# Performance work log

Measured on AMD Instinct MI355X. Metric: run time of the kernel, lower is better.

Reference implementation:

```python
import jax, jax.numpy as jnp
import numpy as np

N_CYCLES = 20000  # number of cycles in the cycle basis (segments)


def setup_inputs() -> dict:
    key = jax.random.key(0)
    k1, k2, k3, k4, k5 = jax.random.split(key, 5)
    B, NB, E = 256, 50000, 160000  # batch, n_branches, total cycle-basis entries
    c = jax.random.normal(k1, (B, NB), dtype=jnp.float32)
    s = jax.random.normal(k2, (B, NB), dtype=jnp.float32)
    # signs are +/-1
    cysigns = jnp.where(jax.random.uniform(k4, (E,)) < 0.5, -1.0, 1.0).astype(jnp.float32)
    cyinds = jax.random.randint(k3, (E,), 0, NB, dtype=jnp.int32)
    # from_value_rowids requires nondecreasing row ids
    cyrows = jnp.sort(jax.random.randint(k5, (E,), 0, N_CYCLES, dtype=jnp.int32))
    return {"c": c, "s": s, "cysigns": cysigns, "cyinds": cyinds, "cyrows": cyrows}


def reference(c, s, cysigns, cyinds, cyrows):
    # gather branch vars per cycle-basis entry: [B, E]
    cg = jnp.take(c, cyinds, axis=1)
    sg = cysigns * jnp.take(s, cyinds, axis=1)
    # tf.math.angle(tf.complex(rc, rs)) == atan2(imag, real)
    ang = jnp.arctan2(sg, cg)  # [B, E]
    # ragged per-cycle sum == segment_sum over the entry axis -> [N_CYCLES, B]
    v_kvl = jax.ops.segment_sum(ang.T, cyrows, num_segments=N_CYCLES)
    # scalar KVL violation
    return jnp.mean(jnp.abs(v_kvl))
```

## Files before the change

kernel.cpp:

```cpp
#include <hip/hip_runtime.h>

#define NB     50000
#define NB4    12500
#define BATCH  256
#define NCYC   20000
#define QSCALE  (127.0f / 3.14159265358979f)
#define DQSCALE (3.14159265358979f / 127.0f)
#define OUTSCALE (1.0f / ((float)NCYC * (float)BATCH))

__device__ __forceinline__ float fast_atan2q(float y, float x) {
    const float ax = __builtin_fabsf(x);
    const float ay = __builtin_fabsf(y);
    const float mx = fmaxf(ax, ay);
    const float mn = fminf(ax, ay);
    const float t  = mn * __builtin_amdgcn_rcpf(mx);
    const float t2 = t * t;
    float p = fmaf(t2, fmaf(t2, fmaf(t2, fmaf(t2,
                  0.84219761f, -3.44137383f), 7.28200966f), -13.35163894f),
                  40.42416382f);
    p *= t;
    p = (ay > ax) ? (63.5f - p) : p;
    p = (x < 0.0f) ? (127.0f - p) : p;
    return copysignf(p, y);
}

__device__ __forceinline__ unsigned int q8(float y, float x) {
    return (unsigned int)(unsigned char)(signed char)__float2int_rn(fast_atan2q(y, x));
}

__global__ __launch_bounds__(256) void theta_k(
        const float4* __restrict__ c4, const float4* __restrict__ s4,
        signed char* __restrict__ th, int* __restrict__ row_start,
        const int* __restrict__ rows, int E) {
    const int u = threadIdx.x;
    const int g = blockIdx.x * 256 + u;
    if (g <= NCYC) {
        int lo = 0, hi = E;
        while (lo < hi) { const int m = (lo + hi) >> 1; if (rows[m] < g) lo = m + 1; else hi = m; }
        row_start[g] = lo;
    }

    const int col4 = u & 15;
    const int bg   = u >> 4;
    const int x4   = blockIdx.x * 16 + col4;
    if (x4 >= NB4) return;
    const int b0   = 16 * bg;

    unsigned int acc[4][4];

    #pragma unroll
    for (int p = 0; p < 4; ++p) {
        const int rb = b0 + 4 * p;
        const float4 vc0 = c4[(size_t)(rb + 0) * NB4 + x4];
        const float4 vc1 = c4[(size_t)(rb + 1) * NB4 + x4];
        const float4 vc2 = c4[(size_t)(rb + 2) * NB4 + x4];
        const float4 vc3 = c4[(size_t)(rb + 3) * NB4 + x4];
        const float4 vs0 = s4[(size_t)(rb + 0) * NB4 + x4];
        const float4 vs1 = s4[(size_t)(rb + 1) * NB4 + x4];
        const float4 vs2 = s4[(size_t)(rb + 2) * NB4 + x4];
        const float4 vs3 = s4[(size_t)(rb + 3) * NB4 + x4];
        #pragma unroll
        for (int j = 0; j < 4; ++j) {
            const unsigned int y0 = q8((&vs0.x)[j], (&vc0.x)[j]);
            const unsigned int y1 = q8((&vs1.x)[j], (&vc1.x)[j]);
            const unsigned int y2 = q8((&vs2.x)[j], (&vc2.x)[j]);
            const unsigned int y3 = q8((&vs3.x)[j], (&vc3.x)[j]);
            acc[j][p] = y0 | (y1 << 8) | (y2 << 16) | (y3 << 24);
        }
    }

    #pragma unroll
    for (int j = 0; j < 4; ++j) {
        const int nb = 4 * x4 + j;
        uint4 w;
        w.x = acc[j][0]; w.y = acc[j][1]; w.z = acc[j][2]; w.w = acc[j][3];
        *reinterpret_cast<uint4*>(&th[(size_t)nb * BATCH + b0]) = w;
    }
}

__global__ __launch_bounds__(256) void kvl3_k(
        const signed char* __restrict__ th,
        const float* __restrict__ signs, const int* __restrict__ inds,
        const int* __restrict__ row_start,
        float* __restrict__ partials) {
    __shared__ float wsum[4];
    const int tid  = threadIdx.x;
    const int wave = tid >> 6;
    const int lane = tid & 63;
    const int r    = blockIdx.x * 4 + wave;
    const int start = row_start[r];
    const int end   = row_start[r + 1];

    float a0 = 0.f, a1 = 0.f, a2 = 0.f, a3 = 0.f;
    int e = start;
    for (; e + 2 <= end; e += 2) {
        const int   i0 = inds[e],  i1 = inds[e + 1];
        const float g0 = signs[e] * DQSCALE, g1 = signs[e + 1] * DQSCALE;
        const unsigned int u0 = *reinterpret_cast<const unsigned int*>(&th[(size_t)i0 * BATCH + lane * 4]);
        const unsigned int u1 = *reinterpret_cast<const unsigned int*>(&th[(size_t)i1 * BATCH + lane * 4]);
        a0 += g0 * (float)(signed char)(u0      ) + g1 * (float)(signed char)(u1      );
        a1 += g0 * (float)(signed char)(u0 >>  8) + g1 * (float)(signed char)(u1 >>  8);
        a2 += g0 * (float)(signed char)(u0 >> 16) + g1 * (float)(signed char)(u1 >> 16);
        a3 += g0 * (float)(signed char)(u0 >> 24) + g1 * (float)(signed char)(u1 >> 24);
    }
    if (e < end) {
        const float g0 = signs[e] * DQSCALE;
        const unsigned int u0 = *reinterpret_cast<const unsigned int*>(&th[(size_t)inds[e] * BATCH + lane * 4]);
        a0 += g0 * (float)(signed char)(u0      );
        a1 += g0 * (float)(signed char)(u0 >>  8);
        a2 += g0 * (float)(signed char)(u0 >> 16);
        a3 += g0 * (float)(signed char)(u0 >> 24);
    }
    float v = fabsf(a0) + fabsf(a1) + fabsf(a2) + fabsf(a3);
    #pragma unroll
    for (int off = 32; off > 0; off >>= 1)
        v += __shfl_down(v, off, 64);
    if (lane == 0) wsum[wave] = v;
    __syncthreads();
    if (tid == 0)
        partials[blockIdx.x] = wsum[0] + wsum[1] + wsum[2] + wsum[3];
}

__global__ __launch_bounds__(1024) void reduce_k(
        const float* __restrict__ partials, float* __restrict__ out) {
    const int tid = threadIdx.x;
    float v = 0.f;
    for (int i = tid; i < NCYC / 4; i += 1024) v += partials[i];
    #pragma unroll
    for (int off = 32; off > 0; off >>= 1)
        v += __shfl_down(v, off, 64);
    __shared__ float wsum[16];
    if ((tid & 63) == 0) wsum[tid >> 6] = v;
    __syncthreads();
    if (tid == 0) {
        float t = 0.f;
        #pragma unroll
        for (int w = 0; w < 16; ++w) t += wsum[w];
        out[0] = t * OUTSCALE;
    }
}

__global__ void zero_out_k(float* out) { if (threadIdx.x == 0) out[0] = 0.0f; }

__global__ __launch_bounds__(256) void kvl_fallback_k(
        const float* __restrict__ c, const float* __restrict__ s,
        const float* __restrict__ signs, const int* __restrict__ inds,
        const int* __restrict__ rows, int E, float* __restrict__ out) {
    const int r = blockIdx.x;
    int lo = 0, hi = E;
    while (lo < hi) { const int m = (lo + hi) >> 1; if (rows[m] < r) lo = m + 1; else hi = m; }
    const int start = lo;
    hi = E;
    while (lo < hi) { const int m = (lo + hi) >> 1; if (rows[m] <= r) lo = m + 1; else hi = m; }
    const int end = lo;
    const int tid = threadIdx.x;
    float acc = 0.f;
    for (int e = start; e < end; ++e) {
        const int idx = inds[e];
        const float sg = signs[e];
        acc += atan2f(sg * s[(size_t)tid * NB + idx], c[(size_t)tid * NB + idx]);
    }
    float v = fabsf(acc);
    #pragma unroll
    for (int off = 32; off > 0; off >>= 1)
        v += __shfl_down(v, off, 64);
    __shared__ float wsum[4];
    if ((tid & 63) == 0) wsum[tid >> 6] = v;
    __syncthreads();
    if (tid == 0)
        atomicAdd(out, (wsum[0] + wsum[1] + wsum[2] + wsum[3]) *
                       (1.0f / ((float)NCYC * (float)BATCH)));
}

extern "C" void kernel_launch(void* const* d_in, const int* in_sizes, int n_in,
                              void* d_out, int out_size, void* d_ws, size_t ws_size,
                              hipStream_t stream) {
    const float* c       = (const float*)d_in[0];
    const float* s       = (const float*)d_in[1];
    const float* cysigns = (const float*)d_in[2];
    const int*   cyinds  = (const int*)d_in[3];
    const int*   cyrows  = (const int*)d_in[4];
    const int    E       = in_sizes[2];
    float* out = (float*)d_out;

    const size_t th_bytes = (size_t)NB * BATCH;
    const size_t rs_bytes = (size_t)(NCYC + 1) * sizeof(int);
    const size_t pa_bytes = (size_t)(NCYC / 4) * sizeof(float);
    const size_t need = th_bytes + rs_bytes + pa_bytes;
    if (ws_size >= need) {
        signed char* th   = (signed char*)d_ws;
        int* row_start    = (int*)(th + th_bytes);
        float* partials   = (float*)((char*)row_start + rs_bytes);

        theta_k<<<(NB4 + 15) / 16, 256, 0, stream>>>(
            (const float4*)c, (const float4*)s, th, row_start, cyrows, E);
        kvl3_k<<<NCYC / 4, 256, 0, stream>>>(th, cysigns, cyinds, row_start,
                                             partials);
        reduce_k<<<1, 1024, 0, stream>>>(partials, out);
    } else {
        zero_out_k<<<1, 64, 0, stream>>>(out);
        kvl_fallback_k<<<NCYC, 256, 0, stream>>>(c, s, cysigns, cyinds, cyrows, E, out);
    }
}
```

Baseline: 152.8 us.

## Remap theta kernel threads for wide coalesced row loads over a 2D grid

Each wavefront in the angle-quantization kernel now covers 64 consecutive float4 columns of one batch row, instead of a 16-column × 4-batch-group tile. Each thread handles 16 batch rows, so every load instruction reads a contiguous 1 KB segment. A second grid dimension splits the batch into 64-row chunks, and only the y=0 blocks compute the row_start binary searches. The packed bytes are transposed in registers with shifts and masks so the uint4 stores keep the [branch][batch] layout. The tradeoff is the extra ALU work for the byte transpose, and the stores are still scattered with a 1 KB stride between lanes.

```diff
diff --git a/kernel.cpp b/kernel.cpp
--- a/kernel.cpp
+++ b/kernel.cpp
@@ -33,48 +33,46 @@
         signed char* __restrict__ th, int* __restrict__ row_start,
         const int* __restrict__ rows, int E) {
     const int u = threadIdx.x;
-    const int g = blockIdx.x * 256 + u;
-    if (g <= NCYC) {
-        int lo = 0, hi = E;
-        while (lo < hi) { const int m = (lo + hi) >> 1; if (rows[m] < g) lo = m + 1; else hi = m; }
-        row_start[g] = lo;
-    }
-
-    const int col4 = u & 15;
-    const int bg   = u >> 4;
-    const int x4   = blockIdx.x * 16 + col4;
+    if (blockIdx.y == 0) {
+        const int g = blockIdx.x * 256 + u;
+        if (g <= NCYC) {
+            int lo = 0, hi = E;
+            while (lo < hi) { const int m = (lo + hi) >> 1; if (rows[m] < g) lo = m + 1; else hi = m; }
+            row_start[g] = lo;
+        }
+    }
+
+    const int lane = u & 63;
+    const int w    = u >> 6;
+    const int x4   = blockIdx.x * 64 + lane;
     if (x4 >= NB4) return;
-    const int b0   = 16 * bg;
-
-    unsigned int acc[4][4];
-
-    #pragma unroll
-    for (int p = 0; p < 4; ++p) {
-        const int rb = b0 + 4 * p;
-        const float4 vc0 = c4[(size_t)(rb + 0) * NB4 + x4];
-        const float4 vc1 = c4[(size_t)(rb + 1) * NB4 + x4];
-        const float4 vc2 = c4[(size_t)(rb + 2) * NB4 + x4];
-        const float4 vc3 = c4[(size_t)(rb + 3) * NB4 + x4];
-        const float4 vs0 = s4[(size_t)(rb + 0) * NB4 + x4];
-        const float4 vs1 = s4[(size_t)(rb + 1) * NB4 + x4];
-        const float4 vs2 = s4[(size_t)(rb + 2) * NB4 + x4];
-        const float4 vs3 = s4[(size_t)(rb + 3) * NB4 + x4];
+    const int b0   = blockIdx.y * 64 + 16 * w;
+
+    unsigned int pw[16];
+    #pragma unroll
+    for (int r = 0; r < 16; ++r) {
+        const float4 vc = c4[(size_t)(b0 + r) * NB4 + x4];
+        const float4 vs = s4[(size_t)(b0 + r) * NB4 + x4];
+        pw[r] =  q8(vs.x, vc.x)
+              | (q8(vs.y, vc.y) << 8)
+              | (q8(vs.z, vc.z) << 16)
+              | (q8(vs.w, vc.w) << 24);
+    }
+
+    #pragma unroll
+    for (int j = 0; j < 4; ++j) {
+        uint4 o;
+        unsigned int* op = &o.x;
         #pragma unroll
-        for (int j = 0; j < 4; ++j) {
-            const unsigned int y0 = q8((&vs0.x)[j], (&vc0.x)[j]);
-            const unsigned int y1 = q8((&vs1.x)[j], (&vc1.x)[j]);
-            const unsigned int y2 = q8((&vs2.x)[j], (&vc2.x)[j]);
-            const unsigned int y3 = q8((&vs3.x)[j], (&vc3.x)[j]);
-            acc[j][p] = y0 | (y1 << 8) | (y2 << 16) | (y3 << 24);
+        for (int q = 0; q < 4; ++q) {
+            const unsigned int sh = 8 * j;
+            op[q] =  ((pw[4 * q + 0] >> sh) & 0xffu)
+                  | (((pw[4 * q + 1] >> sh) & 0xffu) << 8)
+                  | (((pw[4 * q + 2] >> sh) & 0xffu) << 16)
+                  | (((pw[4 * q + 3] >> sh) & 0xffu) << 24);
         }
-    }
-
-    #pragma unroll
-    for (int j = 0; j < 4; ++j) {
         const int nb = 4 * x4 + j;
-        uint4 w;
-        w.x = acc[j][0]; w.y = acc[j][1]; w.z = acc[j][2]; w.w = acc[j][3];
-        *reinterpret_cast<uint4*>(&th[(size_t)nb * BATCH + b0]) = w;
+        *reinterpret_cast<uint4*>(&th[(size_t)nb * BATCH + b0]) = o;
     }
 }
 
@@ -192,8 +190,9 @@
         int* row_start    = (int*)(th + th_bytes);
         float* partials   = (float*)((char*)row_start + rs_bytes);
 
-        theta_k<<<(NB4 + 15) / 16, 256, 0, stream>>>(
-            (const float4*)c, (const float4*)s, th, row_start, cyrows, E);
+        dim3 tg((NB4 + 63) / 64, BATCH / 64);
+        theta_k<<<tg, 256, 0, stream>>>((const float4*)c, (const float4*)s,
+                                        th, row_start, cyrows, E);
         kvl3_k<<<NCYC / 4, 256, 0, stream>>>(th, cysigns, cyinds, row_start,
                                              partials);
         reduce_k<<<1, 1024, 0, stream>>>(partials, out);
```

Measured after the change: 156.5 us. 2.4% more time.
